# Optimization experiments

Measured on AMD Instinct MI355X. Metric: run time of the kernel, lower is better.

Reference implementation:

```python
import jax, jax.numpy as jnp
import numpy as np

B, N, H = 8, 256, 128  # graphs, nodes per graph (equal counts), hidden_dim


def setup_inputs() -> dict:
    key = jax.random.key(0)
    k1, k2, k3, k4, k5, k6 = jax.random.split(key, 6)
    total = B * N
    h = jax.random.normal(k1, (total, H), dtype=jnp.float32)
    pos = jax.random.normal(k2, (total, 3), dtype=jnp.float32)
    # sorted segment ids, equal counts per graph (padding becomes a reshape)
    batch = jnp.repeat(jnp.arange(B, dtype=jnp.int64), N)
    # phi: Linear(2H+1 -> H) -> SiLU -> Linear(H -> 1), torch default init
    s1 = 1.0 / np.sqrt(2 * H + 1)
    s2 = 1.0 / np.sqrt(H)
    W1 = jax.random.uniform(k3, (2 * H + 1, H), minval=-s1, maxval=s1, dtype=jnp.float32)
    b1 = jax.random.uniform(k4, (H,), minval=-s1, maxval=s1, dtype=jnp.float32)
    W2 = jax.random.uniform(k5, (H, 1), minval=-s2, maxval=s2, dtype=jnp.float32)
    b2 = jax.random.uniform(k6, (1,), minval=-s2, maxval=s2, dtype=jnp.float32)
    return {"h": h, "pos": pos, "batch": batch, "W1": W1, "b1": b1, "W2": W2, "b2": b2}


def _safe_norm(diff):
    # exact forward (0 on diagonal), grad-safe (no nan from sqrt at 0)
    sq = jnp.sum(diff * diff, axis=-1, keepdims=True)
    pos_sq = sq > 0
    return jnp.where(pos_sq, jnp.sqrt(jnp.where(pos_sq, sq, 1.0)), 0.0)


def reference(h, pos, batch, W1, b1, W2, b2):
    # batch is sorted with equal counts per graph -> padding == reshape,
    # mask is all-True, so v_pred_padded[mask] == reshape back to [total, 3].
    hp = h.reshape(B, N, H)
    pp = pos.reshape(B, N, 3)

    # diff[b, p, q] = pos[b, q] - pos[b, p]  (matches unsqueeze(1) - unsqueeze(2))
    diff = pp[:, None, :, :] - pp[:, :, None, :]        # [B, N, N, 3]
    dist = _safe_norm(diff)                              # [B, N, N, 1]

    # cat([h_i, h_j, dist]) @ W1 done without materializing the concat:
    # h_i[b,p,q] = h[b,q], h_j[b,p,q] = h[b,p]
    Wa, Wb, wd = W1[:H], W1[H:2 * H], W1[2 * H]
    pre = (hp @ Wa)[:, None, :, :] + (hp @ Wb)[:, :, None, :] + dist * wd + b1
    coeff = jax.nn.silu(pre) @ W2 + b2                   # [B, N, N, 1]

    v = jnp.sum(coeff * diff, axis=2)                    # [B, N, 3]
    return v.reshape(B * N, 3)
```

## Files before the change

kernel.cpp:

```cpp
#include <hip/hip_runtime.h>
#include <math.h>

#define BATCH 8
#define NPTS  256
#define HDIM  128
#define TOTAL (BATCH * NPTS)
#define IT    2

#define NEG_LOG2E -1.4426950408889634f
#define NEG_LN2   -0.6931471805599453f

__global__ __launch_bounds__(HDIM) void evh_prep_kernel(
    const float* __restrict__ h, const float* __restrict__ W1,
    const float* __restrict__ b1, float* __restrict__ A_T4,
    float* __restrict__ Bb)
{
    __shared__ float hrow[HDIM];
    const int t = blockIdx.x;
    const int c = threadIdx.x;
    hrow[c] = h[t * HDIM + c];
    __syncthreads();

    float a = 0.f, bsum = 0.f;
#pragma unroll 8
    for (int k = 0; k < HDIM; ++k) {
        const float hv = hrow[k];
        a    = fmaf(hv, W1[k * HDIM + c], a);
        bsum = fmaf(hv, W1[(HDIM + k) * HDIM + c], bsum);
    }
    A_T4[(c >> 2) * (4 * TOTAL) + 4 * t + (c & 3)] = a * NEG_LOG2E;
    Bb[t * HDIM + c] = (bsum + b1[c]) * NEG_LOG2E;
}

__global__ __launch_bounds__(256) void evh_pair_kernel(
    const float* __restrict__ A_T4, const float* __restrict__ Bb,
    const float* __restrict__ pos, const float* __restrict__ W1,
    const float* __restrict__ W2, const float* __restrict__ b2,
    float* __restrict__ out)
{
    const int blk = blockIdx.x;
    const int b   = blk >> 7;
    const int i0  = (blk & 127) * IT;
    const int tid = threadIdx.x;
    const int brow  = b * NPTS;
    const int row_j = brow + tid;

    __shared__ float4 wdq[HDIM / 4], w2q[HDIM / 4], bbq[IT][HDIM / 4];
    if (tid < 32) {
        const float* wdp = W1 + 2 * HDIM * HDIM;
        const float4 w = *reinterpret_cast<const float4*>(wdp + 4 * tid);
        wdq[tid] = make_float4(w.x * NEG_LOG2E, w.y * NEG_LOG2E,
                               w.z * NEG_LOG2E, w.w * NEG_LOG2E);
        const float4 v = *reinterpret_cast<const float4*>(W2 + 4 * tid);
        w2q[tid] = make_float4(v.x * NEG_LN2, v.y * NEG_LN2,
                               v.z * NEG_LN2, v.w * NEG_LN2);
    } else if (tid < 32 + IT * 32) {
        const int s = (tid - 32) >> 5;
        const int q = (tid - 32) & 31;
        bbq[s][q] = *reinterpret_cast<const float4*>(
                        &Bb[(brow + i0 + s) * HDIM + 4 * q]);
    }

    const float pjx = pos[row_j * 3 + 0];
    const float pjy = pos[row_j * 3 + 1];
    const float pjz = pos[row_j * 3 + 2];

    float dx[IT], dy[IT], dz[IT], dist[IT];
#pragma unroll
    for (int s = 0; s < IT; ++s) {
        const int row_i = brow + i0 + s;
        dx[s] = pjx - pos[row_i * 3 + 0];
        dy[s] = pjy - pos[row_i * 3 + 1];
        dz[s] = pjz - pos[row_i * 3 + 2];
        dist[s] = sqrtf(dx[s] * dx[s] + dy[s] * dy[s] + dz[s] * dz[s]);
    }
    __syncthreads();

    float acc0 = 0.f, acc1 = 0.f;
    const float* aptr = A_T4 + 4 * row_j;

#define CELL(AK, BK, WDK, W2K, ACC, D)                                  \
    {                                                                   \
        const float pre2 = fmaf((D), (WDK), (AK) + (BK));               \
        const float e = __builtin_amdgcn_exp2f(pre2);                   \
        const float r = __builtin_amdgcn_rcpf(1.f + e);                 \
        ACC = fmaf((W2K), pre2 * r, ACC);                               \
    }

#pragma unroll 4
    for (int c4 = 0; c4 < HDIM / 4; ++c4) {
        const float4 a   = *reinterpret_cast<const float4*>(
                               aptr + c4 * (4 * TOTAL));
        const float4 wd  = wdq[c4];
        const float4 w2  = w2q[c4];
        const float4 bb0 = bbq[0][c4];
        const float4 bb1 = bbq[1][c4];

        CELL(a.x, bb0.x, wd.x, w2.x, acc0, dist[0])
        CELL(a.y, bb0.y, wd.y, w2.y, acc0, dist[0])
        CELL(a.z, bb0.z, wd.z, w2.z, acc0, dist[0])
        CELL(a.w, bb0.w, wd.w, w2.w, acc0, dist[0])
        CELL(a.x, bb1.x, wd.x, w2.x, acc1, dist[1])
        CELL(a.y, bb1.y, wd.y, w2.y, acc1, dist[1])
        CELL(a.z, bb1.z, wd.z, w2.z, acc1, dist[1])
        CELL(a.w, bb1.w, wd.w, w2.w, acc1, dist[1])
    }
#undef CELL

    const float b2v  = b2[0];
    const int   wave = tid >> 6;
    const int   lane = tid & 63;
    __shared__ float vsh[4][IT][3];

    float accs[IT] = {acc0, acc1};
#pragma unroll
    for (int s = 0; s < IT; ++s) {
        const float coeff = accs[s] + b2v;
        float vx = coeff * dx[s];
        float vy = coeff * dy[s];
        float vz = coeff * dz[s];
#pragma unroll
        for (int off = 32; off >= 1; off >>= 1) {
            vx += __shfl_xor(vx, off, 64);
            vy += __shfl_xor(vy, off, 64);
            vz += __shfl_xor(vz, off, 64);
        }
        if (lane == 0) {
            vsh[wave][s][0] = vx; vsh[wave][s][1] = vy; vsh[wave][s][2] = vz;
        }
    }
    __syncthreads();
    if (tid < IT * 3) {
        const int s = tid / 3, comp = tid % 3;
        out[(brow + i0 + s) * 3 + comp] =
            vsh[0][s][comp] + vsh[1][s][comp] + vsh[2][s][comp] + vsh[3][s][comp];
    }
}

extern "C" void kernel_launch(void* const* d_in, const int* in_sizes, int n_in,
                              void* d_out, int out_size, void* d_ws, size_t ws_size,
                              hipStream_t stream) {
    const float* h   = (const float*)d_in[0];
    const float* pos = (const float*)d_in[1];
    const float* W1  = (const float*)d_in[3];
    const float* b1  = (const float*)d_in[4];
    const float* W2  = (const float*)d_in[5];
    const float* b2  = (const float*)d_in[6];
    float* out = (float*)d_out;

    float* A_T4 = (float*)d_ws;
    float* Bb   = A_T4 + TOTAL * HDIM;

    evh_prep_kernel<<<TOTAL, HDIM, 0, stream>>>(h, W1, b1, A_T4, Bb);
    evh_pair_kernel<<<TOTAL / IT, 256, 0, stream>>>(A_T4, Bb, pos, W1, W2, b2, out);
}
```

Before: 35.87 us.

## Split hidden dimension across two blocks and combine partial sums with atomics

The pair kernel now launches twice as many blocks, and each handles half of the hidden channels for two query rows. Partial velocity sums are combined with atomicAdd into an output that the prep kernel zeroes. The prescaled wd/W2 vectors are precomputed once in the prep kernel, and Bb/wd/w2 are read directly from global memory instead of being staged in shared memory with a barrier. This is meant to improve occupancy and latency hiding, in exchange for atomics and a dependence on the prep kernel to zero the output.

```diff
diff --git a/kernel.cpp b/kernel.cpp
--- a/kernel.cpp
+++ b/kernel.cpp
@@ -5,20 +5,26 @@
 #define NPTS  256
 #define HDIM  128
 #define TOTAL (BATCH * NPTS)
-#define IT    2
 
 #define NEG_LOG2E -1.4426950408889634f
 #define NEG_LN2   -0.6931471805599453f
 
 __global__ __launch_bounds__(HDIM) void evh_prep_kernel(
     const float* __restrict__ h, const float* __restrict__ W1,
-    const float* __restrict__ b1, float* __restrict__ A_T4,
-    float* __restrict__ Bb)
+    const float* __restrict__ b1, const float* __restrict__ W2,
+    float* __restrict__ A_T4, float* __restrict__ Bb,
+    float* __restrict__ wdx, float* __restrict__ w2x,
+    float* __restrict__ out)
 {
     __shared__ float hrow[HDIM];
     const int t = blockIdx.x;
     const int c = threadIdx.x;
     hrow[c] = h[t * HDIM + c];
+    if (t == 0) {
+        wdx[c] = W1[2 * HDIM * HDIM + c] * NEG_LOG2E;
+        w2x[c] = W2[c] * NEG_LN2;
+    }
+    if (c < 3) out[t * 3 + c] = 0.f;
     __syncthreads();
 
     float a = 0.f, bsum = 0.f;
@@ -34,50 +40,43 @@
 
 __global__ __launch_bounds__(256) void evh_pair_kernel(
     const float* __restrict__ A_T4, const float* __restrict__ Bb,
-    const float* __restrict__ pos, const float* __restrict__ W1,
-    const float* __restrict__ W2, const float* __restrict__ b2,
+    const float* __restrict__ wdx, const float* __restrict__ w2x,
+    const float* __restrict__ pos, const float* __restrict__ b2,
     float* __restrict__ out)
 {
     const int blk = blockIdx.x;
-    const int b   = blk >> 7;
-    const int i0  = (blk & 127) * IT;
+    const int ch  = blk & 1;
+    const int b   = blk >> 8;
+    const int i0  = ((blk >> 1) & 127) * 2;
     const int tid = threadIdx.x;
     const int brow  = b * NPTS;
     const int row_j = brow + tid;
-
-    __shared__ float4 wdq[HDIM / 4], w2q[HDIM / 4], bbq[IT][HDIM / 4];
-    if (tid < 32) {
-        const float* wdp = W1 + 2 * HDIM * HDIM;
-        const float4 w = *reinterpret_cast<const float4*>(wdp + 4 * tid);
-        wdq[tid] = make_float4(w.x * NEG_LOG2E, w.y * NEG_LOG2E,
-                               w.z * NEG_LOG2E, w.w * NEG_LOG2E);
-        const float4 v = *reinterpret_cast<const float4*>(W2 + 4 * tid);
-        w2q[tid] = make_float4(v.x * NEG_LN2, v.y * NEG_LN2,
-                               v.z * NEG_LN2, v.w * NEG_LN2);
-    } else if (tid < 32 + IT * 32) {
-        const int s = (tid - 32) >> 5;
-        const int q = (tid - 32) & 31;
-        bbq[s][q] = *reinterpret_cast<const float4*>(
-                        &Bb[(brow + i0 + s) * HDIM + 4 * q]);
-    }
 
     const float pjx = pos[row_j * 3 + 0];
     const float pjy = pos[row_j * 3 + 1];
     const float pjz = pos[row_j * 3 + 2];
 
-    float dx[IT], dy[IT], dz[IT], dist[IT];
-#pragma unroll
-    for (int s = 0; s < IT; ++s) {
-        const int row_i = brow + i0 + s;
-        dx[s] = pjx - pos[row_i * 3 + 0];
-        dy[s] = pjy - pos[row_i * 3 + 1];
-        dz[s] = pjz - pos[row_i * 3 + 2];
-        dist[s] = sqrtf(dx[s] * dx[s] + dy[s] * dy[s] + dz[s] * dz[s]);
+    float dx0, dy0, dz0, dist0, dx1, dy1, dz1, dist1;
+    {
+        const int r0 = brow + i0, r1 = r0 + 1;
+        dx0 = pjx - pos[r0 * 3 + 0];
+        dy0 = pjy - pos[r0 * 3 + 1];
+        dz0 = pjz - pos[r0 * 3 + 2];
+        dist0 = sqrtf(dx0 * dx0 + dy0 * dy0 + dz0 * dz0);
+        dx1 = pjx - pos[r1 * 3 + 0];
+        dy1 = pjy - pos[r1 * 3 + 1];
+        dz1 = pjz - pos[r1 * 3 + 2];
+        dist1 = sqrtf(dx1 * dx1 + dy1 * dy1 + dz1 * dz1);
     }
-    __syncthreads();
+
+    const float* __restrict__ bb0p = Bb + (size_t)(brow + i0) * HDIM + ch * 64;
+    const float* __restrict__ bb1p = bb0p + HDIM;
+    const float* __restrict__ wdp  = wdx + ch * 64;
+    const float* __restrict__ w2p  = w2x + ch * 64;
+    const float* __restrict__ ap   = A_T4 + 4 * row_j
+                                     + (size_t)(ch * 16) * (4 * TOTAL);
 
     float acc0 = 0.f, acc1 = 0.f;
-    const float* aptr = A_T4 + 4 * row_j;
 
 #define CELL(AK, BK, WDK, W2K, ACC, D)                                  \
     {                                                                   \
@@ -88,52 +87,53 @@
     }
 
 #pragma unroll 4
-    for (int c4 = 0; c4 < HDIM / 4; ++c4) {
-        const float4 a   = *reinterpret_cast<const float4*>(
-                               aptr + c4 * (4 * TOTAL));
-        const float4 wd  = wdq[c4];
-        const float4 w2  = w2q[c4];
-        const float4 bb0 = bbq[0][c4];
-        const float4 bb1 = bbq[1][c4];
+    for (int q = 0; q < 16; ++q) {
+        const float4 a  = *reinterpret_cast<const float4*>(
+                              ap + (size_t)q * (4 * TOTAL));
+        const float4 b0 = *reinterpret_cast<const float4*>(bb0p + 4 * q);
+        const float4 b1 = *reinterpret_cast<const float4*>(bb1p + 4 * q);
+        const float4 wd = *reinterpret_cast<const float4*>(wdp + 4 * q);
+        const float4 w2 = *reinterpret_cast<const float4*>(w2p + 4 * q);
 
-        CELL(a.x, bb0.x, wd.x, w2.x, acc0, dist[0])
-        CELL(a.y, bb0.y, wd.y, w2.y, acc0, dist[0])
-        CELL(a.z, bb0.z, wd.z, w2.z, acc0, dist[0])
-        CELL(a.w, bb0.w, wd.w, w2.w, acc0, dist[0])
-        CELL(a.x, bb1.x, wd.x, w2.x, acc1, dist[1])
-        CELL(a.y, bb1.y, wd.y, w2.y, acc1, dist[1])
-        CELL(a.z, bb1.z, wd.z, w2.z, acc1, dist[1])
-        CELL(a.w, bb1.w, wd.w, w2.w, acc1, dist[1])
+        CELL(a.x, b0.x, wd.x, w2.x, acc0, dist0)
+        CELL(a.y, b0.y, wd.y, w2.y, acc0, dist0)
+        CELL(a.z, b0.z, wd.z, w2.z, acc0, dist0)
+        CELL(a.w, b0.w, wd.w, w2.w, acc0, dist0)
+        CELL(a.x, b1.x, wd.x, w2.x, acc1, dist1)
+        CELL(a.y, b1.y, wd.y, w2.y, acc1, dist1)
+        CELL(a.z, b1.z, wd.z, w2.z, acc1, dist1)
+        CELL(a.w, b1.w, wd.w, w2.w, acc1, dist1)
     }
 #undef CELL
 
-    const float b2v  = b2[0];
-    const int   wave = tid >> 6;
-    const int   lane = tid & 63;
-    __shared__ float vsh[4][IT][3];
+    const float cext = (ch == 0) ? b2[0] : 0.f;
+    const int wave = tid >> 6;
+    const int lane = tid & 63;
 
-    float accs[IT] = {acc0, acc1};
+    const float c0 = acc0 + cext;
+    const float c1 = acc1 + cext;
+    float v0x = c0 * dx0, v0y = c0 * dy0, v0z = c0 * dz0;
+    float v1x = c1 * dx1, v1y = c1 * dy1, v1z = c1 * dz1;
 #pragma unroll
-    for (int s = 0; s < IT; ++s) {
-        const float coeff = accs[s] + b2v;
-        float vx = coeff * dx[s];
-        float vy = coeff * dy[s];
-        float vz = coeff * dz[s];
-#pragma unroll
-        for (int off = 32; off >= 1; off >>= 1) {
-            vx += __shfl_xor(vx, off, 64);
-            vy += __shfl_xor(vy, off, 64);
-            vz += __shfl_xor(vz, off, 64);
-        }
-        if (lane == 0) {
-            vsh[wave][s][0] = vx; vsh[wave][s][1] = vy; vsh[wave][s][2] = vz;
-        }
+    for (int off = 32; off >= 1; off >>= 1) {
+        v0x += __shfl_xor(v0x, off, 64);
+        v0y += __shfl_xor(v0y, off, 64);
+        v0z += __shfl_xor(v0z, off, 64);
+        v1x += __shfl_xor(v1x, off, 64);
+        v1y += __shfl_xor(v1y, off, 64);
+        v1z += __shfl_xor(v1z, off, 64);
+    }
+
+    __shared__ float vsh[4][6];
+    if (lane == 0) {
+        vsh[wave][0] = v0x; vsh[wave][1] = v0y; vsh[wave][2] = v0z;
+        vsh[wave][3] = v1x; vsh[wave][4] = v1y; vsh[wave][5] = v1z;
     }
     __syncthreads();
-    if (tid < IT * 3) {
+    if (tid < 6) {
+        const float val = vsh[0][tid] + vsh[1][tid] + vsh[2][tid] + vsh[3][tid];
         const int s = tid / 3, comp = tid % 3;
-        out[(brow + i0 + s) * 3 + comp] =
-            vsh[0][s][comp] + vsh[1][s][comp] + vsh[2][s][comp] + vsh[3][s][comp];
+        atomicAdd(&out[(brow + i0 + s) * 3 + comp], val);
     }
 }
 
@@ -150,7 +150,11 @@
 
     float* A_T4 = (float*)d_ws;
     float* Bb   = A_T4 + TOTAL * HDIM;
+    float* wdx  = Bb + TOTAL * HDIM;
+    float* w2x  = wdx + HDIM;
 
-    evh_prep_kernel<<<TOTAL, HDIM, 0, stream>>>(h, W1, b1, A_T4, Bb);
-    evh_pair_kernel<<<TOTAL / IT, 256, 0, stream>>>(A_T4, Bb, pos, W1, W2, b2, out);
+    evh_prep_kernel<<<TOTAL, HDIM, 0, stream>>>(h, W1, b1, W2,
+                                                A_T4, Bb, wdx, w2x, out);
+    evh_pair_kernel<<<TOTAL, 256, 0, stream>>>(A_T4, Bb, wdx, w2x,
+                                               pos, b2, out);
 }
```

Result: faster. 33.67 us (-6.1%).
